# Kernel optimization log

Measured on AMD Instinct MI355X. Metric: run time of the kernel, lower is better.

## Reference

```python
import jax, jax.numpy as jnp
import numpy as np

B, T, C = 2, 2048, 1024
H = 16
D = C // H          # head_dim = 64
WIN = 256           # local window


def _rope(x):
    # x: [B, H, T, D]; rotate pairs (even, odd) with per-pair frequencies.
    t = x.shape[2]
    d = x.shape[-1] // 2
    theta = 10000.0 ** (-(jnp.arange(d, dtype=x.dtype) / d))          # [d]
    ang = jnp.arange(t, dtype=x.dtype)[:, None] * theta               # [T, d]
    sin, cos = jnp.sin(ang), jnp.cos(ang)                             # [T, d]
    x1, x2 = x[..., ::2], x[..., 1::2]                                # [B,H,T,d]
    out = jnp.stack([x1 * cos - x2 * sin, x1 * sin + x2 * cos], axis=-1)
    return out.reshape(x.shape)


def setup_inputs() -> dict:
    key = jax.random.key(0)
    k1, k2, k3 = jax.random.split(key, 3)
    s = 1.0 / np.sqrt(C)
    return {
        "x": jax.random.normal(k1, (B, T, C), dtype=jnp.float32),
        "w_qkv": jax.random.normal(k2, (3 * C, C), dtype=jnp.float32) * s,
        "w_out": jax.random.normal(k3, (C, C), dtype=jnp.float32) * s,
        "b_out": jnp.zeros((C,), dtype=jnp.float32),
    }


def reference(x, w_qkv, w_out, b_out):
    b, t, c = x.shape
    qkv = x @ w_qkv.T                                   # [B,T,3C]
    qkv = qkv.reshape(b, t, H, 3 * D).transpose(0, 2, 1, 3)  # [B,H,T,3D]
    q, k, v = jnp.split(qkv, 3, axis=-1)                # each [B,H,T,D]
    q, k = _rope(q), _rope(k)
    scores = jnp.einsum("bhqd,bhkd->bhqk", q, k) / jnp.sqrt(jnp.asarray(D, x.dtype))
    i = jnp.arange(t)[:, None]
    j = jnp.arange(t)[None, :]
    mask = (j <= i) & (j >= i - WIN)                    # causal local window
    scores = jnp.where(mask, scores, -jnp.inf)
    attn = jax.nn.softmax(scores, axis=-1)              # [B,H,T,T]
    out = jnp.einsum("bhqk,bhkd->bhqd", attn, v)        # [B,H,T,D]
    out = out.transpose(0, 2, 1, 3).reshape(b, t, c)    # [B,T,C]
    return out @ w_out.T + b_out
```

## Files before the change

### kernel.cpp

```cpp
#include <hip/hip_runtime.h>
#include <math.h>

#define BB 2
#define TT 2048
#define CC 1024
#define HH 16
#define DD 64
#define WINW 256

constexpr int MROWS  = BB * TT;
constexpr int NQKV   = 3 * CC;
constexpr int QKV_LD = 3 * CC;

typedef unsigned short ushort_t;
typedef __attribute__((ext_vector_type(8))) short  bf16x8;
typedef __attribute__((ext_vector_type(4))) float  f32x4;
typedef __attribute__((ext_vector_type(8))) unsigned short u16x8;

__device__ __forceinline__ float bf2f(ushort_t u) {
    return __uint_as_float(((unsigned int)u) << 16);
}
__device__ __forceinline__ ushort_t f2bf(float f) {
    unsigned int u = __float_as_uint(f);
    u += 0x7fffu + ((u >> 16) & 1u);
    return (ushort_t)(u >> 16);
}

__device__ __forceinline__ void async16(void* lds, const void* g) {
    __builtin_amdgcn_global_load_lds(
        (const __attribute__((address_space(1))) unsigned int*)g,
        (__attribute__((address_space(3))) unsigned int*)lds, 16, 0, 0);
}

#define ROPE_LN 0.2878231366242557f

constexpr int NX = MROWS * CC;
constexpr int NQ = NQKV * CC;
constexpr int NO = CC * CC;

__global__ __launch_bounds__(256)
void convert_all(const float* __restrict__ x, const float* __restrict__ wq,
                 const float* __restrict__ wo, ushort_t* __restrict__ xb,
                 ushort_t* __restrict__ wqb, ushort_t* __restrict__ wob) {
    int i = (blockIdx.x * 256 + threadIdx.x) * 4;
    const float* src;
    ushort_t* dst;
    if (i < NX)           { src = x  + i;             dst = xb  + i; }
    else if (i < NX + NQ) { src = wq + (i - NX);      dst = wqb + (i - NX); }
    else                  { src = wo + (i - NX - NQ); dst = wob + (i - NX - NQ); }
    float4 v = *(const float4*)src;
    ushort4 o;
    o.x = f2bf(v.x); o.y = f2bf(v.y); o.z = f2bf(v.z); o.w = f2bf(v.w);
    *(ushort4*)dst = o;
}

__global__ __launch_bounds__(512)
void gemm1_8phase(const ushort_t* __restrict__ A, const ushort_t* __restrict__ Bw,
                  ushort_t* __restrict__ Cc) {
    constexpr int K = 1024, N = 3072, NT = 16;
    __shared__ __align__(16) ushort_t As[2][2][256 * 32];
    __shared__ __align__(16) ushort_t Bs[2][2][256 * 32];

    const int tid  = threadIdx.x;
    const int lane = tid & 63;
    const int w    = tid >> 6;
    const int wm   = w >> 2;
    const int wn   = w & 3;
    const int fr   = lane & 15;
    const int fq   = lane >> 4;

    const int nbx = NQKV / 256;
    int flat = blockIdx.y * nbx + blockIdx.x;
    flat = (flat & 7) * 24 + (flat >> 3);
    const int bm = (flat / nbx) * 256;
    const int bn = (flat % nbx) * 256;

    const int sr  = tid >> 2;
    const int dcb = tid & 3;
    const int scb = dcb ^ ((sr >> 1) & 3);

    const int cbr = fq ^ ((fr >> 1) & 3);

    f32x4 acc[8][4];
#pragma unroll
    for (int m = 0; m < 8; ++m)
#pragma unroll
        for (int n = 0; n < 4; ++n)
            acc[m][n] = f32x4{0.f, 0.f, 0.f, 0.f};

#pragma unroll
    for (int p = 0; p < 4; ++p) {
        const int skh = p >> 1;
        const bool isB = p & 1;
        const ushort_t* G = isB ? Bw : A;
        const int br = isB ? bn : bm;
        ushort_t* L = isB ? &Bs[0][skh][0] : &As[0][skh][0];
#pragma unroll
        for (int hh = 0; hh < 2; ++hh)
            async16(&L[(hh * 128 + sr) * 32 + dcb * 8],
                    G + (size_t)(br + hh * 128 + sr) * K + skh * 32 + scb * 8);
    }

    for (int t = 0; t < NT; ++t) {
        const int d  = t & 1;
        const int tn = (t + 1) & (NT - 1);
        bf16x8 bfr[4];

#pragma unroll
        for (int ph = 0; ph < 4; ++ph) {
            const int kh = ph >> 1;
            const int mh = ph & 1;

            {
                const int skh = ph >> 1;
                const bool isB = ph & 1;
                const ushort_t* G = isB ? Bw : A;
                const int br = isB ? bn : bm;
                ushort_t* L = isB ? &Bs[d ^ 1][skh][0] : &As[d ^ 1][skh][0];
#pragma unroll
                for (int hh = 0; hh < 2; ++hh)
                    async16(&L[(hh * 128 + sr) * 32 + dcb * 8],
                            G + (size_t)(br + hh * 128 + sr) * K
                              + (size_t)tn * 64 + skh * 32 + scb * 8);
            }

            if (mh == 0)
                asm volatile("s_waitcnt vmcnt(6)" ::: "memory");
            __builtin_amdgcn_s_barrier();
            __builtin_amdgcn_sched_barrier(0);

            if (mh == 0) {
#pragma unroll
                for (int n = 0; n < 4; ++n) {
                    const int rb = wn * 64 + n * 16 + fr;
                    bfr[n] = *(const bf16x8*)&Bs[d][kh][rb * 32 + cbr * 8];
                }
            }
            bf16x8 afr[4];
#pragma unroll
            for (int i = 0; i < 4; ++i) {
                const int ra = wm * 128 + (mh * 4 + i) * 16 + fr;
                afr[i] = *(const bf16x8*)&As[d][kh][ra * 32 + cbr * 8];
            }

            __builtin_amdgcn_s_setprio(1);
#pragma unroll
            for (int i = 0; i < 4; ++i)
#pragma unroll
                for (int n = 0; n < 4; ++n)
                    acc[mh * 4 + i][n] = __builtin_amdgcn_mfma_f32_16x16x32_bf16(
                        afr[i], bfr[n], acc[mh * 4 + i][n], 0, 0, 0);
            __builtin_amdgcn_s_setprio(0);
            __builtin_amdgcn_s_barrier();
        }
    }

#pragma unroll
    for (int m = 0; m < 8; ++m)
#pragma unroll
        for (int n = 0; n < 4; ++n)
#pragma unroll
            for (int j = 0; j < 4; ++j) {
                const int row = bm + wm * 128 + m * 16 + fq * 4 + j;
                const int col = bn + wn * 64 + n * 16 + fr;
                Cc[(size_t)row * N + col] = f2bf(acc[m][n][j]);
            }
}

template <bool BIAS, bool OUT_BF16>
__global__ __launch_bounds__(256)
void gemm_nt_mfma(const ushort_t* __restrict__ A, const ushort_t* __restrict__ Bw,
                  const float* __restrict__ bias, void* __restrict__ Cc,
                  int M, int N, int K) {
    __shared__ __align__(16) ushort_t As[128 * 32];
    __shared__ __align__(16) ushort_t Bs[128 * 32];

    const int tid  = threadIdx.x;
    const int lane = tid & 63;
    const int wv   = tid >> 6;
    const int wr   = wv >> 1;
    const int wc   = wv & 1;
    const int bm   = blockIdx.y * 128;
    const int bn   = blockIdx.x * 128;

    const int srow = tid >> 2;
    const int scol = (tid & 3) * 8;

    const ushort_t* Ag = A + (size_t)(bm + srow) * K + scol;
    const ushort_t* Bg = Bw + (size_t)(bn + srow) * K + scol;

    f32x4 acc[4][4];
#pragma unroll
    for (int m = 0; m < 4; ++m)
#pragma unroll
        for (int n = 0; n < 4; ++n)
            acc[m][n] = f32x4{0.f, 0.f, 0.f, 0.f};

    const int fr = lane & 15;
    const int fq = lane >> 4;

    for (int k0 = 0; k0 < K; k0 += 32) {
        async16(&As[tid * 8],        Ag);
        async16(&As[2048 + tid * 8], Ag + (size_t)64 * K);
        async16(&Bs[tid * 8],        Bg);
        async16(&Bs[2048 + tid * 8], Bg + (size_t)64 * K);
        Ag += 32; Bg += 32;
        __syncthreads();

        bf16x8 af[4], bfv[4];
#pragma unroll
        for (int m = 0; m < 4; ++m)
            af[m] = *(const bf16x8*)&As[(wr * 64 + m * 16 + fr) * 32 + fq * 8];
#pragma unroll
        for (int n = 0; n < 4; ++n)
            bfv[n] = *(const bf16x8*)&Bs[(wc * 64 + n * 16 + fr) * 32 + fq * 8];
#pragma unroll
        for (int m = 0; m < 4; ++m)
#pragma unroll
            for (int n = 0; n < 4; ++n)
                acc[m][n] = __builtin_amdgcn_mfma_f32_16x16x32_bf16(
                    af[m], bfv[n], acc[m][n], 0, 0, 0);
        __syncthreads();
    }

#pragma unroll
    for (int m = 0; m < 4; ++m) {
#pragma unroll
        for (int n = 0; n < 4; ++n) {
            const int col = bn + wc * 64 + n * 16 + fr;
            const float bv = BIAS ? bias[col] : 0.0f;
#pragma unroll
            for (int j = 0; j < 4; ++j) {
                const int row = bm + wr * 64 + m * 16 + fq * 4 + j;
                float v = acc[m][n][j] + bv;
                if (OUT_BF16)
                    ((ushort_t*)Cc)[(size_t)row * N + col] = f2bf(v);
                else
                    ((float*)Cc)[(size_t)row * N + col] = v;
            }
        }
    }
}

#define MASKNEG (-1e30f)

__global__ __launch_bounds__(512)
void attn_mfma(const ushort_t* __restrict__ qkv, ushort_t* __restrict__ out) {
    __shared__ __align__(16) ushort_t Ks[2][64 * 64];
    __shared__ __align__(16) ushort_t Vlin[2][64 * 64];
    __shared__ __align__(16) ushort_t Vt[64 * 72];
    __shared__ __align__(16) ushort_t Ps[8][16 * 72];

    const int tid  = threadIdx.x;
    const int lane = tid & 63;
    const int w    = tid >> 6;
    const int fr   = lane & 15;
    const int fq   = lane >> 4;

    const int blk = blockIdx.x;
    const int qt  = blk & 15;
    const int h   = (blk >> 4) & 15;
    const int b   = blk >> 8;
    const int q0  = qt * 128;

    const ushort_t* base = qkv + (size_t)(b * TT) * QKV_LD + h * (3 * DD);

    const int srow = tid >> 3;
    const int cbs  = (tid & 7) ^ (srow & 7);

    float thK[4];
#pragma unroll
    for (int e = 0; e < 4; ++e)
        thK[e] = __expf(-ROPE_LN * (float)(cbs * 4 + e));

    bf16x8 qf0, qf1;
    {
        const int tq = q0 + w * 16 + fr;
        const ushort_t* qrow = base + (size_t)tq * QKV_LD;
        u16x8 r0 = *(const u16x8*)(qrow + fq * 8);
        u16x8 r1 = *(const u16x8*)(qrow + 32 + fq * 8);
        const float tf = (float)tq;
#pragma unroll
        for (int e = 0; e < 4; ++e) {
            float th0 = __expf(-ROPE_LN * (float)(fq * 4 + e));
            float a0 = tf * th0;
            float s0 = __sinf(a0), c0 = __cosf(a0);
            float x1 = bf2f(r0[2 * e]), x2 = bf2f(r0[2 * e + 1]);
            r0[2 * e]     = f2bf(x1 * c0 - x2 * s0);
            r0[2 * e + 1] = f2bf(x1 * s0 + x2 * c0);
            float th1 = __expf(-ROPE_LN * (float)(16 + fq * 4 + e));
            float a1 = tf * th1;
            float s1 = __sinf(a1), c1 = __cosf(a1);
            float y1 = bf2f(r1[2 * e]), y2 = bf2f(r1[2 * e + 1]);
            r1[2 * e]     = f2bf(y1 * c1 - y2 * s1);
            r1[2 * e + 1] = f2bf(y1 * s1 + y2 * c1);
        }
        qf0 = *(bf16x8*)&r0;
        qf1 = *(bf16x8*)&r1;
    }

    f32x4 oacc[4];
#pragma unroll
    for (int nd = 0; nd < 4; ++nd) oacc[nd] = f32x4{0.f, 0.f, 0.f, 0.f};
    float mj[4], lj[4];
#pragma unroll
    for (int j = 0; j < 4; ++j) { mj[j] = MASKNEG; lj[j] = 0.f; }

    const int kstart = (q0 >= WINW) ? (q0 - WINW) : 0;
    const int ntiles = (q0 + 128 - kstart) >> 6;

    {
        const ushort_t* src = base + (size_t)(kstart + srow) * QKV_LD + DD + cbs * 8;
        u16x8 kv = *(const u16x8*)src;
        const float tf = (float)(kstart + srow);
#pragma unroll
        for (int e = 0; e < 4; ++e) {
            float a = tf * thK[e];
            float s = __sinf(a), c = __cosf(a);
            float x1 = bf2f(kv[2 * e]), x2 = bf2f(kv[2 * e + 1]);
            kv[2 * e]     = f2bf(x1 * c - x2 * s);
            kv[2 * e + 1] = f2bf(x1 * s + x2 * c);
        }
        *(u16x8*)&Ks[0][tid * 8] = kv;
        async16(&Vlin[0][tid * 8], src + DD);
    }
    __syncthreads();

    int cur = 0;
    for (int t = 0; t < ntiles; ++t) {
        const int kt0 = kstart + t * 64;
        const bool pf = (t + 1 < ntiles);

        u16x8 kpre;
        if (pf) {
            const ushort_t* src =
                base + (size_t)(kt0 + 64 + srow) * QKV_LD + DD + cbs * 8;
            kpre = *(const u16x8*)src;
            async16(&Vlin[cur ^ 1][tid * 8], src + DD);
        }

        {
            u16x8 vv = *(const u16x8*)&Vlin[cur][lane * 64 + ((w ^ (lane & 7)) * 8)];
#pragma unroll
            for (int e = 0; e < 8; ++e)
                Vt[(w * 8 + e) * 72 + lane] = vv[e];
        }

        f32x4 s[4];
#pragma unroll
        for (int n = 0; n < 4; ++n) {
            const int krow = n * 16 + fr;
            bf16x8 kb0 = *(const bf16x8*)&Ks[cur][krow * 64 + ((fq ^ (krow & 7)) * 8)];
            bf16x8 kb1 = *(const bf16x8*)&Ks[cur][krow * 64 + (((fq + 4) ^ (krow & 7)) * 8)];
            f32x4 z = f32x4{0.f, 0.f, 0.f, 0.f};
            z = __builtin_amdgcn_mfma_f32_16x16x32_bf16(qf0, kb0, z, 0, 0, 0);
            s[n] = __builtin_amdgcn_mfma_f32_16x16x32_bf16(qf1, kb1, z, 0, 0, 0);
        }

        float pmax[4];
#pragma unroll
        for (int j = 0; j < 4; ++j) pmax[j] = MASKNEG;
#pragma unroll
        for (int n = 0; n < 4; ++n) {
            const int key = kt0 + n * 16 + fr;
#pragma unroll
            for (int j = 0; j < 4; ++j) {
                const int qi = q0 + w * 16 + fq * 4 + j;
                const bool ok = (key <= qi) && (key >= qi - WINW);
                float sv = ok ? s[n][j] * 0.125f : MASKNEG;
                s[n][j] = sv;
                pmax[j] = fmaxf(pmax[j], sv);
            }
        }
#pragma unroll
        for (int off = 1; off < 16; off <<= 1)
#pragma unroll
            for (int j = 0; j < 4; ++j)
                pmax[j] = fmaxf(pmax[j], __shfl_xor(pmax[j], off));

        float tl[4] = {0.f, 0.f, 0.f, 0.f};
#pragma unroll
        for (int j = 0; j < 4; ++j) {
            float mnew = fmaxf(mj[j], pmax[j]);
            float alpha = (mnew <= -1e29f) ? 1.0f : __expf(mj[j] - mnew);
            mj[j] = mnew;
            lj[j] *= alpha;
#pragma unroll
            for (int nd = 0; nd < 4; ++nd) oacc[nd][j] *= alpha;
        }
#pragma unroll
        for (int n = 0; n < 4; ++n) {
#pragma unroll
            for (int j = 0; j < 4; ++j) {
                float sv = s[n][j];
                float p = (sv <= -1e29f) ? 0.f : __expf(sv - mj[j]);
                tl[j] += p;
                Ps[w][(fq * 4 + j) * 72 + n * 16 + fr] = f2bf(p);
            }
        }
#pragma unroll
        for (int off = 1; off < 16; off <<= 1)
#pragma unroll
            for (int j = 0; j < 4; ++j)
                tl[j] += __shfl_xor(tl[j], off);
#pragma unroll
        for (int j = 0; j < 4; ++j) lj[j] += tl[j];

        if (pf) {
            const float tf = (float)(kt0 + 64 + srow);
#pragma unroll
            for (int e = 0; e < 4; ++e) {
                float a = tf * thK[e];
                float s2 = __sinf(a), c2 = __cosf(a);
                float x1 = bf2f(kpre[2 * e]), x2 = bf2f(kpre[2 * e + 1]);
                kpre[2 * e]     = f2bf(x1 * c2 - x2 * s2);
                kpre[2 * e + 1] = f2bf(x1 * s2 + x2 * c2);
            }
            *(u16x8*)&Ks[cur ^ 1][tid * 8] = kpre;
        }

        __syncthreads();

        bf16x8 pa0 = *(const bf16x8*)&Ps[w][fr * 72 + fq * 8];
        bf16x8 pa1 = *(const bf16x8*)&Ps[w][fr * 72 + 32 + fq * 8];
#pragma unroll
        for (int nd = 0; nd < 4; ++nd) {
            bf16x8 vb0 = *(const bf16x8*)&Vt[(nd * 16 + fr) * 72 + fq * 8];
            bf16x8 vb1 = *(const bf16x8*)&Vt[(nd * 16 + fr) * 72 + 32 + fq * 8];
            oacc[nd] = __builtin_amdgcn_mfma_f32_16x16x32_bf16(pa0, vb0, oacc[nd], 0, 0, 0);
            oacc[nd] = __builtin_amdgcn_mfma_f32_16x16x32_bf16(pa1, vb1, oacc[nd], 0, 0, 0);
        }

        __syncthreads();
        cur ^= 1;
    }

#pragma unroll
    for (int nd = 0; nd < 4; ++nd) {
#pragma unroll
        for (int j = 0; j < 4; ++j) {
            const int qi = q0 + w * 16 + fq * 4 + j;
            out[(size_t)(b * TT + qi) * CC + h * DD + nd * 16 + fr] =
                f2bf(oacc[nd][j] / lj[j]);
        }
    }
}

extern "C" void kernel_launch(void* const* d_in, const int* in_sizes, int n_in,
                              void* d_out, int out_size, void* d_ws, size_t ws_size,
                              hipStream_t stream) {
    const float* x     = (const float*)d_in[0];
    const float* w_qkv = (const float*)d_in[1];
    const float* w_out = (const float*)d_in[2];
    const float* b_out = (const float*)d_in[3];
    float* out = (float*)d_out;

    ushort_t* qkv_b  = (ushort_t*)d_ws;
    ushort_t* attn_b = qkv_b  + (size_t)MROWS * NQKV;
    ushort_t* xb     = attn_b + (size_t)MROWS * CC;
    ushort_t* wqb    = xb     + (size_t)MROWS * CC;
    ushort_t* wob    = wqb    + (size_t)NQKV * CC;

    convert_all<<<(NX + NQ + NO) / 1024, 256, 0, stream>>>(
        x, w_qkv, w_out, xb, wqb, wob);

    gemm1_8phase<<<dim3(NQKV / 256, MROWS / 256), 512, 0, stream>>>(
        xb, wqb, qkv_b);

    attn_mfma<<<BB * HH * (TT / 128), 512, 0, stream>>>(qkv_b, attn_b);

    gemm_nt_mfma<true, false><<<dim3(CC / 128, MROWS / 128), 256, 0, stream>>>(
        attn_b, wob, b_out, out, MROWS, CC, CC);
}
```

Before: 108.9 us.

## Skip fully masked attention tiles per wave, swizzle GEMM blocks, prefetch A fragments

The attention kernel now checks whether each wave's 16-query slice overlaps the current 64-key tile. If it does not, the wave skips the QK MFMAs, the softmax update and the PV MFMAs, removing wasted work at the window edges. The output-projection GEMM remaps block indices with an XCD-style swizzle so neighbouring tiles land on the same die for better L2 reuse. The pipelined QKV GEMM issues its second-half A fragment loads before the barrier and drops a sched_barrier, letting LDS reads overlap synchronisation.

```diff
diff --git a/kernel.cpp b/kernel.cpp
--- a/kernel.cpp
+++ b/kernel.cpp
@@ -124,10 +124,17 @@
                               + (size_t)tn * 64 + skh * 32 + scb * 8);
             }
 
-            if (mh == 0)
+            bf16x8 afr[4];
+            if (mh == 1) {
+#pragma unroll
+                for (int i = 0; i < 4; ++i) {
+                    const int ra = wm * 128 + (4 + i) * 16 + fr;
+                    afr[i] = *(const bf16x8*)&As[d][kh][ra * 32 + cbr * 8];
+                }
+            } else {
                 asm volatile("s_waitcnt vmcnt(6)" ::: "memory");
+            }
             __builtin_amdgcn_s_barrier();
-            __builtin_amdgcn_sched_barrier(0);
 
             if (mh == 0) {
 #pragma unroll
@@ -135,12 +142,11 @@
                     const int rb = wn * 64 + n * 16 + fr;
                     bfr[n] = *(const bf16x8*)&Bs[d][kh][rb * 32 + cbr * 8];
                 }
-            }
-            bf16x8 afr[4];
-#pragma unroll
-            for (int i = 0; i < 4; ++i) {
-                const int ra = wm * 128 + (mh * 4 + i) * 16 + fr;
-                afr[i] = *(const bf16x8*)&As[d][kh][ra * 32 + cbr * 8];
+#pragma unroll
+                for (int i = 0; i < 4; ++i) {
+                    const int ra = wm * 128 + i * 16 + fr;
+                    afr[i] = *(const bf16x8*)&As[d][kh][ra * 32 + cbr * 8];
+                }
             }
 
             __builtin_amdgcn_s_setprio(1);
@@ -180,8 +186,13 @@
     const int wv   = tid >> 6;
     const int wr   = wv >> 1;
     const int wc   = wv & 1;
-    const int bm   = blockIdx.y * 128;
-    const int bn   = blockIdx.x * 128;
+
+    const int nbx = gridDim.x;
+    const int nwg = nbx * gridDim.y;
+    int flat = blockIdx.y * nbx + blockIdx.x;
+    flat = (flat & 7) * (nwg >> 3) + (flat >> 3);
+    const int bm = (flat / nbx) * 128;
+    const int bn = (flat % nbx) * 128;
 
     const int srow = tid >> 2;
     const int scol = (tid & 3) * 8;
@@ -308,6 +319,7 @@
 
     const int kstart = (q0 >= WINW) ? (q0 - WINW) : 0;
     const int ntiles = (q0 + 128 - kstart) >> 6;
+    const int qlo = q0 + w * 16;
 
     {
         const ushort_t* src = base + (size_t)(kstart + srow) * QKV_LD + DD + cbs * 8;
@@ -330,6 +342,7 @@
     for (int t = 0; t < ntiles; ++t) {
         const int kt0 = kstart + t * 64;
         const bool pf = (t + 1 < ntiles);
+        const bool act = (kt0 <= qlo + 15) && (kt0 + 63 >= qlo - WINW);
 
         u16x8 kpre;
         if (pf) {
@@ -346,65 +359,67 @@
                 Vt[(w * 8 + e) * 72 + lane] = vv[e];
         }
 
-        f32x4 s[4];
-#pragma unroll
-        for (int n = 0; n < 4; ++n) {
-            const int krow = n * 16 + fr;
-            bf16x8 kb0 = *(const bf16x8*)&Ks[cur][krow * 64 + ((fq ^ (krow & 7)) * 8)];
-            bf16x8 kb1 = *(const bf16x8*)&Ks[cur][krow * 64 + (((fq + 4) ^ (krow & 7)) * 8)];
-            f32x4 z = f32x4{0.f, 0.f, 0.f, 0.f};
-            z = __builtin_amdgcn_mfma_f32_16x16x32_bf16(qf0, kb0, z, 0, 0, 0);
-            s[n] = __builtin_amdgcn_mfma_f32_16x16x32_bf16(qf1, kb1, z, 0, 0, 0);
-        }
-
-        float pmax[4];
-#pragma unroll
-        for (int j = 0; j < 4; ++j) pmax[j] = MASKNEG;
-#pragma unroll
-        for (int n = 0; n < 4; ++n) {
-            const int key = kt0 + n * 16 + fr;
+        if (act) {
+            f32x4 s[4];
+#pragma unroll
+            for (int n = 0; n < 4; ++n) {
+                const int krow = n * 16 + fr;
+                bf16x8 kb0 = *(const bf16x8*)&Ks[cur][krow * 64 + ((fq ^ (krow & 7)) * 8)];
+                bf16x8 kb1 = *(const bf16x8*)&Ks[cur][krow * 64 + (((fq + 4) ^ (krow & 7)) * 8)];
+                f32x4 z = f32x4{0.f, 0.f, 0.f, 0.f};
+                z = __builtin_amdgcn_mfma_f32_16x16x32_bf16(qf0, kb0, z, 0, 0, 0);
+                s[n] = __builtin_amdgcn_mfma_f32_16x16x32_bf16(qf1, kb1, z, 0, 0, 0);
+            }
+
+            float pmax[4];
+#pragma unroll
+            for (int j = 0; j < 4; ++j) pmax[j] = MASKNEG;
+#pragma unroll
+            for (int n = 0; n < 4; ++n) {
+                const int key = kt0 + n * 16 + fr;
+#pragma unroll
+                for (int j = 0; j < 4; ++j) {
+                    const int qi = qlo + fq * 4 + j;
+                    const bool ok = (key <= qi) && (key >= qi - WINW);
+                    float sv = ok ? s[n][j] * 0.125f : MASKNEG;
+                    s[n][j] = sv;
+                    pmax[j] = fmaxf(pmax[j], sv);
+                }
+            }
+#pragma unroll
+            for (int off = 1; off < 16; off <<= 1)
+#pragma unroll
+                for (int j = 0; j < 4; ++j)
+                    pmax[j] = fmaxf(pmax[j], __shfl_xor(pmax[j], off));
+
+            float tl[4] = {0.f, 0.f, 0.f, 0.f};
 #pragma unroll
             for (int j = 0; j < 4; ++j) {
-                const int qi = q0 + w * 16 + fq * 4 + j;
-                const bool ok = (key <= qi) && (key >= qi - WINW);
-                float sv = ok ? s[n][j] * 0.125f : MASKNEG;
-                s[n][j] = sv;
-                pmax[j] = fmaxf(pmax[j], sv);
-            }
-        }
-#pragma unroll
-        for (int off = 1; off < 16; off <<= 1)
-#pragma unroll
-            for (int j = 0; j < 4; ++j)
-                pmax[j] = fmaxf(pmax[j], __shfl_xor(pmax[j], off));
-
-        float tl[4] = {0.f, 0.f, 0.f, 0.f};
-#pragma unroll
-        for (int j = 0; j < 4; ++j) {
-            float mnew = fmaxf(mj[j], pmax[j]);
-            float alpha = (mnew <= -1e29f) ? 1.0f : __expf(mj[j] - mnew);
-            mj[j] = mnew;
-            lj[j] *= alpha;
-#pragma unroll
-            for (int nd = 0; nd < 4; ++nd) oacc[nd][j] *= alpha;
-        }
-#pragma unroll
-        for (int n = 0; n < 4; ++n) {
-#pragma unroll
-            for (int j = 0; j < 4; ++j) {
-                float sv = s[n][j];
-                float p = (sv <= -1e29f) ? 0.f : __expf(sv - mj[j]);
-                tl[j] += p;
-                Ps[w][(fq * 4 + j) * 72 + n * 16 + fr] = f2bf(p);
-            }
-        }
-#pragma unroll
-        for (int off = 1; off < 16; off <<= 1)
-#pragma unroll
-            for (int j = 0; j < 4; ++j)
-                tl[j] += __shfl_xor(tl[j], off);
-#pragma unroll
-        for (int j = 0; j < 4; ++j) lj[j] += tl[j];
+                float mnew = fmaxf(mj[j], pmax[j]);
+                float alpha = (mnew <= -1e29f) ? 1.0f : __expf(mj[j] - mnew);
+                mj[j] = mnew;
+                lj[j] *= alpha;
+#pragma unroll
+                for (int nd = 0; nd < 4; ++nd) oacc[nd][j] *= alpha;
+            }
+#pragma unroll
+            for (int n = 0; n < 4; ++n) {
+#pragma unroll
+                for (int j = 0; j < 4; ++j) {
+                    float sv = s[n][j];
+                    float p = (sv <= -1e29f) ? 0.f : __expf(sv - mj[j]);
+                    tl[j] += p;
+                    Ps[w][(fq * 4 + j) * 72 + n * 16 + fr] = f2bf(p);
+                }
+            }
+#pragma unroll
+            for (int off = 1; off < 16; off <<= 1)
+#pragma unroll
+                for (int j = 0; j < 4; ++j)
+                    tl[j] += __shfl_xor(tl[j], off);
+#pragma unroll
+            for (int j = 0; j < 4; ++j) lj[j] += tl[j];
+        }
 
         if (pf) {
             const float tf = (float)(kt0 + 64 + srow);
@@ -421,14 +436,16 @@
 
         __syncthreads();
 
-        bf16x8 pa0 = *(const bf16x8*)&Ps[w][fr * 72 + fq * 8];
-        bf16x8 pa1 = *(const bf16x8*)&Ps[w][fr * 72 + 32 + fq * 8];
-#pragma unroll
-        for (int nd = 0; nd < 4; ++nd) {
-            bf16x8 vb0 = *(const bf16x8*)&Vt[(nd * 16 + fr) * 72 + fq * 8];
-            bf16x8 vb1 = *(const bf16x8*)&Vt[(nd * 16 + fr) * 72 + 32 + fq * 8];
-            oacc[nd] = __builtin_amdgcn_mfma_f32_16x16x32_bf16(pa0, vb0, oacc[nd], 0, 0, 0);
-            oacc[nd] = __builtin_amdgcn_mfma_f32_16x16x32_bf16(pa1, vb1, oacc[nd], 0, 0, 0);
+        if (act) {
+            bf16x8 pa0 = *(const bf16x8*)&Ps[w][fr * 72 + fq * 8];
+            bf16x8 pa1 = *(const bf16x8*)&Ps[w][fr * 72 + 32 + fq * 8];
+#pragma unroll
+            for (int nd = 0; nd < 4; ++nd) {
+                bf16x8 vb0 = *(const bf16x8*)&Vt[(nd * 16 + fr) * 72 + fq * 8];
+                bf16x8 vb1 = *(const bf16x8*)&Vt[(nd * 16 + fr) * 72 + 32 + fq * 8];
+                oacc[nd] = __builtin_amdgcn_mfma_f32_16x16x32_bf16(pa0, vb0, oacc[nd], 0, 0, 0);
+                oacc[nd] = __builtin_amdgcn_mfma_f32_16x16x32_bf16(pa1, vb1, oacc[nd], 0, 0, 0);
+            }
         }
 
         __syncthreads();
@@ -439,7 +456,7 @@
     for (int nd = 0; nd < 4; ++nd) {
 #pragma unroll
         for (int j = 0; j < 4; ++j) {
-            const int qi = q0 + w * 16 + fq * 4 + j;
+            const int qi = qlo + fq * 4 + j;
             out[(size_t)(b * TT + qi) * CC + h * DD + nd * 16 + fr] =
                 f2bf(oacc[nd][j] / lj[j]);
         }
```

After: 112.2 us. 1.03x slower.
